# Performance work log

Hardware: AMD Instinct MI355X
Metric: run time of the kernel (lower is better)

The kernel has to match this reference:

```python
import math
import jax, jax.numpy as jnp
import numpy as np

N_HEADS = 16
THETA = 10000.0


def _rope_cos_sin(S, head_dim):
    half = head_dim // 2
    inv_freq = 1.0 / (THETA ** (jnp.arange(half, dtype=jnp.float32) / half))
    t = jnp.arange(S, dtype=jnp.float32)
    freqs = t[:, None] * inv_freq[None, :]  # [S, half]
    return jnp.cos(freqs), jnp.sin(freqs)


def _apply_rope(x, cos, sin):
    # x: [B, H, S, D] float32; cos/sin: [S, D//2]
    half = x.shape[-1] // 2
    x1, x2 = x[..., :half], x[..., half:]
    c = cos[None, None, :, :]
    s = sin[None, None, :, :]
    return jnp.concatenate([x1 * c - x2 * s, x1 * s + x2 * c], axis=-1)


def setup_inputs() -> dict:
    key = jax.random.key(0)
    k1, k2, k3 = jax.random.split(key, 3)
    B, S, D = 4, 2048, 1024
    x = jax.random.normal(k1, (B, S, D), dtype=jnp.float32)
    w_qkv = jax.random.normal(k2, (3 * D, D), dtype=jnp.float32) * (1.0 / math.sqrt(D))
    w_out = jax.random.normal(k3, (D, D), dtype=jnp.float32) * (1.0 / math.sqrt(D))
    return {"x": x, "w_qkv": w_qkv, "w_out": w_out}


def reference(x, w_qkv, w_out):
    B, S, D = x.shape
    H = N_HEADS
    hd = D // H

    qkv = x @ w_qkv.T  # [B, S, 3D]
    q, k, v = jnp.split(qkv, 3, axis=-1)

    def reshape(t):
        return t.reshape(B, S, H, hd).transpose(0, 2, 1, 3)  # [B,H,S,hd]

    q, k, v = reshape(q), reshape(k), reshape(v)

    cos, sin = _rope_cos_sin(S, hd)
    q = _apply_rope(q.astype(jnp.float32), cos, sin).astype(x.dtype)
    k = _apply_rope(k.astype(jnp.float32), cos, sin).astype(x.dtype)

    scale = math.sqrt(hd)
    scores = jnp.einsum("bhsd,bhtd->bhst", q, k) / scale  # [B,H,S,S]
    causal = jnp.tril(jnp.ones((S, S), dtype=bool))
    scores = jnp.where(causal[None, None], scores, -jnp.inf)
    attn = jax.nn.softmax(scores.astype(jnp.float32), axis=-1).astype(x.dtype)

    out = jnp.einsum("bhst,bhtd->bhsd", attn, v)  # [B,H,S,hd]
    out = out.transpose(0, 2, 1, 3).reshape(B, S, D)
    return out @ w_out.T
```

## Files before the change

kernel.cpp:

```cpp
#include <hip/hip_runtime.h>
#include <hip/hip_bf16.h>

#define DEV static __device__ __forceinline__

typedef unsigned short u16;
typedef unsigned int u32;
typedef __attribute__((ext_vector_type(8))) short short8;
typedef __attribute__((ext_vector_type(4))) float f32x4;
typedef __attribute__((ext_vector_type(16))) float f32x16;
typedef __attribute__((ext_vector_type(4))) u32 u32x4;

static constexpr int Bsz = 4, Ssz = 2048, Dsz = 1024, Hn = 16, HD = 64;
static constexpr int Mrows = Bsz * Ssz;

DEV u16 f2bu(float f) {
  union { float f; u32 u; } a; a.f = f;
  u32 u = a.u;
  u32 r = (u + 0x7FFFu + ((u >> 16) & 1u)) >> 16;
  return (u16)r;
}
DEV float b2f(u16 v) {
  union { u32 u; float f; } a; a.u = ((u32)v) << 16;
  return a.f;
}
DEV u32 pk2(float lo, float hi2) {
  __hip_bfloat162 t = __float22bfloat162_rn(make_float2(lo, hi2));
  u32 r; __builtin_memcpy(&r, &t, 4); return r;
}
DEV f32x16 mfma3232(short8 a, short8 b, f32x16 c) {
  return __builtin_amdgcn_mfma_f32_32x32x16_bf16(a, b, c, 0, 0, 0);
}
DEV float max3f(float a, float b, float c) { return fmaxf(fmaxf(a, b), c); }
DEV float ex2(float x) { return __builtin_amdgcn_exp2f(x); }

__global__ void k_cast(const float4* __restrict__ in, ushort4* __restrict__ out, int n4) {
  int stride = gridDim.x * blockDim.x;
  for (int i = blockIdx.x * blockDim.x + threadIdx.x; i < n4; i += stride) {
    float4 v = in[i];
    ushort4 o;
    o.x = f2bu(v.x); o.y = f2bu(v.y); o.z = f2bu(v.z); o.w = f2bu(v.w);
    out[i] = o;
  }
}

__global__ void k_ropetab(float2* __restrict__ cst) {
  int i = blockIdx.x * blockDim.x + threadIdx.x;
  if (i >= Ssz * 32) return;
  int s = i >> 5, d = i & 31;
  float inv = powf(10000.0f, -(float)d / 32.0f);
  float fr = (float)s * inv;
  cst[i] = make_float2(cosf(fr), sinf(fr));
}

DEV void cp16(const u16* g, u16* l) {
  __builtin_amdgcn_global_load_lds((const __attribute__((address_space(1))) u32*)g,
                                   (__attribute__((address_space(3))) u32*)l, 16, 0, 0);
}

template <bool OUTBF16>
__global__ __launch_bounds__(256, 2) void k_gemm(const u16* __restrict__ A,
                                                 const u16* __restrict__ W,
                                                 void* __restrict__ C, int N, int K,
                                                 const float2* __restrict__ cst, int cpx,
                                                 u16* __restrict__ vtp) {
  __shared__ __align__(16) u16 SMEM[33792];
  const int tid = threadIdx.x;
  const int wid = tid >> 6, lane = tid & 63;
  const int lr = lane & 15, u = lane >> 4;
  const int wm = wid >> 1, wn = wid & 1;

  const int wg = blockIdx.x;
  const int xcd = wg & 7;
  const int j = wg >> 3;
  const int brow = (j / cpx) * 128;
  const int bcol = (xcd * cpx + j % cpx) * 128;

  const int rw = wid * 32 + (lane >> 3);
  const int octS = ((lane & 7) ^ (rw & 7)) * 8;
  const u16* aS = A + (size_t)(brow + rw) * K + octS;
  const u16* bS = W + (size_t)(bcol + rw) * K + octS;
  const int dBase = wid * 2048 + lane * 8;

  const int aBase = (wm * 64 + lr) * 64;
  const int bBase = (wn * 64 + lr) * 64;
  const int o0 = (u ^ (lane & 7)) * 8;
  const int o1 = ((4 + u) ^ (lane & 7)) * 8;

  f32x4 acc[4][4];
#pragma unroll
  for (int i = 0; i < 4; ++i)
#pragma unroll
    for (int j2 = 0; j2 < 4; ++j2) acc[i][j2] = (f32x4){0.f, 0.f, 0.f, 0.f};

  const int nt = K >> 6;

#define STG(kk, bb)                                                    \
  do {                                                                 \
    u16* ad = SMEM + (bb)*8192 + dBase;                                \
    u16* bd = SMEM + 16384 + (bb)*8192 + dBase;                        \
    cp16(aS + (kk), ad);                                               \
    cp16(aS + (size_t)8 * K + (kk), ad + 512);                         \
    cp16(aS + (size_t)16 * K + (kk), ad + 1024);                       \
    cp16(aS + (size_t)24 * K + (kk), ad + 1536);                       \
    cp16(bS + (kk), bd);                                               \
    cp16(bS + (size_t)8 * K + (kk), bd + 512);                         \
    cp16(bS + (size_t)16 * K + (kk), bd + 1024);                       \
    cp16(bS + (size_t)24 * K + (kk), bd + 1536);                       \
  } while (0)

  STG(0, 0);

  for (int t = 0; t < nt; ++t) {
    asm volatile("s_waitcnt vmcnt(0)" ::: "memory");
    __builtin_amdgcn_s_barrier();
    if (t + 1 < nt) STG((t + 1) << 6, (t + 1) & 1);
    const u16* ab = SMEM + (t & 1) * 8192;
    const u16* bb = SMEM + 16384 + (t & 1) * 8192;
    short8 a0[4], a1[4], b0[4], b1[4];
#pragma unroll
    for (int mr = 0; mr < 4; ++mr) {
      a0[mr] = *(const short8*)(ab + aBase + mr * 1024 + o0);
      a1[mr] = *(const short8*)(ab + aBase + mr * 1024 + o1);
    }
#pragma unroll
    for (int nr = 0; nr < 4; ++nr) {
      b0[nr] = *(const short8*)(bb + bBase + nr * 1024 + o0);
      b1[nr] = *(const short8*)(bb + bBase + nr * 1024 + o1);
    }
    __builtin_amdgcn_s_setprio(1);
#pragma unroll
    for (int mr = 0; mr < 4; ++mr)
#pragma unroll
      for (int nr = 0; nr < 4; ++nr)
        acc[mr][nr] =
            __builtin_amdgcn_mfma_f32_16x16x32_bf16(a0[mr], b0[nr], acc[mr][nr], 0, 0, 0);
#pragma unroll
    for (int mr = 0; mr < 4; ++mr)
#pragma unroll
      for (int nr = 0; nr < 4; ++nr)
        acc[mr][nr] =
            __builtin_amdgcn_mfma_f32_16x16x32_bf16(a1[mr], b1[nr], acc[mr][nr], 0, 0, 0);
    __builtin_amdgcn_s_setprio(0);
  }
#undef STG

  if (OUTBF16) {
    __syncthreads();
    const int rmode = (bcol < 1024) ? 0 : (bcol < 2048) ? 1 : 2;
    if (rmode < 2) {
      const float sc = (rmode == 0) ? 0.18033688f : 1.0f;
#pragma unroll
      for (int mr = 0; mr < 4; ++mr)
#pragma unroll
        for (int r = 0; r < 4; ++r) {
          const int row = wm * 64 + mr * 16 + u * 4 + r;
          const int s = (brow + row) & 2047;
          const float2 c0 = cst[s * 32 + lr];
          const float2 c1 = cst[s * 32 + 16 + lr];
          const float x10 = acc[mr][0][r], x11 = acc[mr][1][r];
          const float x20 = acc[mr][2][r], x21 = acc[mr][3][r];
          u16* lp = SMEM + row * 136 + wn * 64 + lr;
          lp[0]  = f2bu((x10 * c0.x - x20 * c0.y) * sc);
          lp[16] = f2bu((x11 * c1.x - x21 * c1.y) * sc);
          lp[32] = f2bu((x10 * c0.y + x20 * c0.x) * sc);
          lp[48] = f2bu((x11 * c1.y + x21 * c1.x) * sc);
        }
      __syncthreads();
      u16* cp = (u16*)C;
#pragma unroll
      for (int i = 0; i < 8; ++i) {
        const int e = i * 2048 + tid * 8;
        const int row = e >> 7, col = e & 127;
        short8 v = *(const short8*)(SMEM + row * 136 + col);
        *(short8*)(cp + (size_t)(brow + row) * N + bcol + col) = v;
      }
    } else {
#pragma unroll
      for (int mr = 0; mr < 4; ++mr)
#pragma unroll
        for (int nr = 0; nr < 4; ++nr)
#pragma unroll
          for (int r = 0; r < 4; ++r) {
            const int dl = wn * 64 + nr * 16 + lr;
            const int sl = wm * 64 + mr * 16 + u * 4 + r;
            SMEM[dl * 136 + sl] = f2bu(acc[mr][nr][r]);
          }
      __syncthreads();
      const int bb2 = brow >> 11;
      const int sbase = brow & 2047;
#pragma unroll
      for (int i = 0; i < 8; ++i) {
        const int e = i * 2048 + tid * 8;
        const int dl = e >> 7, sl = e & 127;
        const int gd = (bcol - 2048) + dl;
        short8 v = *(const short8*)(SMEM + dl * 136 + sl);
        *(short8*)(vtp + (size_t)(bb2 * 1024 + gd) * 2048 + sbase + sl) = v;
      }
    }
  } else {
    __syncthreads();
    float* FS = (float*)SMEM;
#pragma unroll
    for (int mr = 0; mr < 4; ++mr)
#pragma unroll
      for (int nr = 0; nr < 4; ++nr)
#pragma unroll
        for (int r = 0; r < 4; ++r)
          FS[(wm * 64 + mr * 16 + u * 4 + r) * 132 + wn * 64 + nr * 16 + lr] =
              acc[mr][nr][r];
    __syncthreads();
    float* cp = (float*)C;
#pragma unroll
    for (int i = 0; i < 16; ++i) {
      const int e = i * 1024 + tid * 4;
      const int row = e >> 7, col = e & 127;
      float4 v = *(const float4*)(FS + row * 132 + col);
      *(float4*)(cp + (size_t)(brow + row) * N + bcol + col) = v;
    }
  }
}

__global__ __launch_bounds__(512, 4) void k_attn(const u16* __restrict__ qkv,
                                                 const u16* __restrict__ vt,
                                                 u16* __restrict__ obuf) {
  __shared__ __align__(16) u16 Ksm[2][64 * 64];
  __shared__ __align__(16) u16 Vsm[2][64 * 64];

  const int tid = threadIdx.x;
  const int wid = tid >> 6;
  const int lane = tid & 63;
  const int l31 = lane & 31;
  const int hi = lane >> 5;
  const int r7 = l31 & 7;

  const int fid = blockIdx.x;
  const int bh = fid & 63;
  const int e = (fid >> 6) & 7;
  const int qt = (e < 4) ? e : (7 - (e & 3));

  const int b = bh >> 4;
  const int h = bh & 15;

  const float NEG = -__builtin_inff();

  const int srow = lane >> 3;
  const int scol = ((lane & 7) ^ srow) * 8;
  const u16* ksrc = qkv + (size_t)(b * Ssz + wid * 8 + srow) * 3072 + 1024 + h * 64 + scol;
  const u16* vsrc = vt + ((size_t)bh * 64 + wid * 8 + srow) * Ssz + scol;
  u16* kD0 = Ksm[0] + wid * 512;
  u16* vD0 = Vsm[0] + wid * 512;

  const int q0 = qt * 256;
  const int qrow = q0 + (wid << 5) + l31;

  const u16* qptr = qkv + (size_t)(b * Ssz + qrow) * 3072 + h * 64 + hi * 8;
  short8 qf[4];
#pragma unroll
  for (int s = 0; s < 4; ++s) qf[s] = *(const short8*)(qptr + s * 16);

  f32x16 o0 = {0.f}, o1 = {0.f};
  float m = NEG, lsum = 0.f;

  const int ntiles = 4 * qt + 4;
  const int lastT = 4 * qt + (wid >> 1);

  cp16(ksrc, kD0);
  cp16(vsrc, vD0);

  const u16* kS = ksrc + (size_t)64 * 3072;
  const u16* vS = vsrc + 64;

  for (int t = 0; t < ntiles; ++t) {
    __syncthreads();
    if (t + 1 < ntiles) {
      const int nb = (t + 1) & 1;
      cp16(kS, kD0 + nb * 4096);
      cp16(vS, vD0 + nb * 4096);
      kS += (size_t)64 * 3072;
      vS += 64;
    }
    if (t > lastT) continue;

    const u16* kbuf = Ksm[t & 1];
    const u16* vbuf = Vsm[t & 1];
    const int kv0 = t << 6;

    f32x16 st0 = {0.f}, st1 = {0.f};
    __builtin_amdgcn_s_setprio(1);
#pragma unroll
    for (int s = 0; s < 4; ++s) {
      const int slot = (((2 * s + hi) ^ r7) << 3);
      short8 k0 = *(const short8*)(kbuf + l31 * 64 + slot);
      short8 k1 = *(const short8*)(kbuf + (32 + l31) * 64 + slot);
      st0 = mfma3232(k0, qf[s], st0);
      st1 = mfma3232(k1, qf[s], st1);
    }
    __builtin_amdgcn_s_setprio(0);

    if (t == lastT) {
      const int kb0 = kv0 + 4 * hi;
#pragma unroll
      for (int r = 0; r < 16; ++r) {
        const int ko = (r & 3) + 8 * (r >> 2);
        if (kb0 + ko > qrow) st0[r] = NEG;
        if (kb0 + 32 + ko > qrow) st1[r] = NEG;
      }
    }

    float c0 = max3f(st0[0], st0[1], st0[2]);
    c0 = max3f(c0, st0[3], st1[0]);
    c0 = max3f(c0, st1[1], st1[2]);
    c0 = fmaxf(c0, st1[3]);
    float c1 = max3f(st0[4], st0[5], st0[6]);
    c1 = max3f(c1, st0[7], st1[4]);
    c1 = max3f(c1, st1[5], st1[6]);
    c1 = fmaxf(c1, st1[7]);
    float c2 = max3f(st0[8], st0[9], st0[10]);
    c2 = max3f(c2, st0[11], st1[8]);
    c2 = max3f(c2, st1[9], st1[10]);
    c2 = fmaxf(c2, st1[11]);
    float c3 = max3f(st0[12], st0[13], st0[14]);
    c3 = max3f(c3, st0[15], st1[12]);
    c3 = max3f(c3, st1[13], st1[14]);
    c3 = fmaxf(c3, st1[15]);
    float pm = fmaxf(max3f(c0, c1, c2), c3);
    pm = fmaxf(pm, __shfl_xor(pm, 32));

    if (!__all(pm <= m + 8.0f)) {
      const float mn = fmaxf(m, pm);
      const float corr = ex2(m - mn);
      lsum *= corr;
      o0 *= corr;
      o1 *= corr;
      m = mn;
    }

    float rsp[4] = {0.f, 0.f, 0.f, 0.f};
#pragma unroll
    for (int r = 0; r < 16; ++r) {
      const float p0 = ex2(st0[r] - m);
      const float p1 = ex2(st1[r] - m);
      st0[r] = p0;
      st1[r] = p1;
      rsp[r & 3] += p0 + p1;
    }
    float rs = (rsp[0] + rsp[1]) + (rsp[2] + rsp[3]);
    rs += __shfl_xor(rs, 32);
    lsum += rs;

    u32 wa[8], wb[8];
#pragma unroll
    for (int g = 0; g < 4; ++g) {
      wa[g] = pk2(st0[4 * g + 0], st0[4 * g + 1]);
      wb[g] = pk2(st0[4 * g + 2], st0[4 * g + 3]);
      wa[4 + g] = pk2(st1[4 * g + 0], st1[4 * g + 1]);
      wb[4 + g] = pk2(st1[4 * g + 2], st1[4 * g + 3]);
    }

#pragma unroll
    for (int s = 0; s < 4; ++s) {
      const u32 uA0 = wa[2 * s], uA1 = wa[2 * s + 1];
      const u32 uB0 = wb[2 * s], uB1 = wb[2 * s + 1];
      const u32 tA0 = __shfl_xor(uA0, 32), tA1 = __shfl_xor(uA1, 32);
      const u32 tB0 = __shfl_xor(uB0, 32), tB1 = __shfl_xor(uB1, 32);
      u32x4 pw;
      pw.x = hi ? tA1 : uA0;
      pw.y = hi ? tB1 : uB0;
      pw.z = hi ? uA1 : tA0;
      pw.w = hi ? uB1 : tB0;
      short8 pfrag = *(short8*)&pw;
      const int slot = (((2 * s + hi) ^ r7) << 3);
      short8 v0 = *(const short8*)(vbuf + l31 * 64 + slot);
      short8 v1 = *(const short8*)(vbuf + (32 + l31) * 64 + slot);
      __builtin_amdgcn_s_setprio(1);
      o0 = mfma3232(v0, pfrag, o0);
      o1 = mfma3232(v1, pfrag, o1);
      __builtin_amdgcn_s_setprio(0);
    }
  }

  const float inv = 1.0f / lsum;
  u16* orow = obuf + (size_t)(b * Ssz + qrow) * 1024 + h * 64;
#pragma unroll
  for (int j = 0; j < 4; ++j) {
    ushort4 s0, s1;
    s0.x = f2bu(o0[4 * j + 0] * inv);
    s0.y = f2bu(o0[4 * j + 1] * inv);
    s0.z = f2bu(o0[4 * j + 2] * inv);
    s0.w = f2bu(o0[4 * j + 3] * inv);
    s1.x = f2bu(o1[4 * j + 0] * inv);
    s1.y = f2bu(o1[4 * j + 1] * inv);
    s1.z = f2bu(o1[4 * j + 2] * inv);
    s1.w = f2bu(o1[4 * j + 3] * inv);
    *(ushort4*)(orow + 8 * j + 4 * hi) = s0;
    *(ushort4*)(orow + 32 + 8 * j + 4 * hi) = s1;
  }
}

extern "C" void kernel_launch(void* const* d_in, const int* in_sizes, int n_in,
                              void* d_out, int out_size, void* d_ws, size_t ws_size,
                              hipStream_t stream) {
  const float* x = (const float*)d_in[0];
  const float* wqkv = (const float*)d_in[1];
  const float* wout = (const float*)d_in[2];

  char* ws = (char*)d_ws;
  u16* xb      = (u16*)(ws + 0);
  u16* wqkvb   = (u16*)(ws + 16777216);
  u16* woutb   = (u16*)(ws + 23068672);
  u16* qkv     = (u16*)(ws + 25165824);
  u16* vt      = (u16*)(ws + 75497472);
  u16* obuf    = (u16*)(ws + 92274688);
  float2* cst  = (float2*)(ws + 109051904);

  k_cast<<<2048, 256, 0, stream>>>((const float4*)x, (ushort4*)xb, Mrows * Dsz / 4);
  k_cast<<<2048, 256, 0, stream>>>((const float4*)wqkv, (ushort4*)wqkvb, 3 * Dsz * Dsz / 4);
  k_cast<<<1024, 256, 0, stream>>>((const float4*)wout, (ushort4*)woutb, Dsz * Dsz / 4);
  k_ropetab<<<256, 256, 0, stream>>>(cst);

  k_gemm<true><<<1536, 256, 0, stream>>>(xb, wqkvb, qkv, 3072, 1024, cst, 3, vt);

  k_attn<<<512, 512, 0, stream>>>(qkv, vt, obuf);

  k_gemm<false><<<512, 256, 0, stream>>>(obuf, woutb, d_out, 1024, 1024, nullptr, 1, nullptr);
}
```

Measured before the change: 182.3 us.

## Split attention KV range across two wave groups with smaller query tiles

```diff
diff --git a/kernel.cpp b/kernel.cpp
--- a/kernel.cpp
+++ b/kernel.cpp
@@ -220,11 +220,10 @@
   }
 }
 
-__global__ __launch_bounds__(512, 4) void k_attn(const u16* __restrict__ qkv,
+__global__ __launch_bounds__(512, 8) void k_attn(const u16* __restrict__ qkv,
                                                  const u16* __restrict__ vt,
                                                  u16* __restrict__ obuf) {
-  __shared__ __align__(16) u16 Ksm[2][64 * 64];
-  __shared__ __align__(16) u16 Vsm[2][64 * 64];
+  __shared__ __align__(16) u16 SM[16384];
 
   const int tid = threadIdx.x;
   const int wid = tid >> 6;
@@ -233,10 +232,14 @@
   const int hi = lane >> 5;
   const int r7 = l31 & 7;
 
+  const int p = wid >> 2;
+  const int s4 = wid & 3;
+
   const int fid = blockIdx.x;
-  const int bh = fid & 63;
-  const int e = (fid >> 6) & 7;
-  const int qt = (e < 4) ? e : (7 - (e & 3));
+  const int a = fid & 3, bq = (fid >> 8) & 3;
+  const int bh = (fid >> 2) & 63;
+  const int sel = a ^ bq;
+  const int qt = (sel == 0) ? bq : (sel == 1) ? 7 - bq : (sel == 2) ? 8 + bq : 15 - bq;
 
   const int b = bh >> 4;
   const int h = bh & 15;
@@ -245,13 +248,15 @@
 
   const int srow = lane >> 3;
   const int scol = ((lane & 7) ^ srow) * 8;
-  const u16* ksrc = qkv + (size_t)(b * Ssz + wid * 8 + srow) * 3072 + 1024 + h * 64 + scol;
-  const u16* vsrc = vt + ((size_t)bh * 64 + wid * 8 + srow) * Ssz + scol;
-  u16* kD0 = Ksm[0] + wid * 512;
-  u16* vD0 = Vsm[0] + wid * 512;
-
-  const int q0 = qt * 256;
-  const int qrow = q0 + (wid << 5) + l31;
+  const u16* kS = qkv + (size_t)(b * Ssz + p * 64 + 16 * s4 + srow) * 3072 + 1024 + h * 64 + scol;
+  const u16* vS = vt + ((size_t)bh * 64 + 16 * s4 + srow) * Ssz + p * 64 + scol;
+  u16* kD = SM + p * 4096 + s4 * 1024;
+  u16* vD = SM + 8192 + p * 4096 + s4 * 1024;
+  const u16* kbuf = SM + p * 4096;
+  const u16* vbuf = SM + 8192 + p * 4096;
+
+  const int q0 = qt * 128;
+  const int qrow = q0 + (s4 << 5) + l31;
 
   const u16* qptr = qkv + (size_t)(b * Ssz + qrow) * 3072 + h * 64 + hi * 8;
   short8 qf[4];
@@ -261,139 +266,165 @@
   f32x16 o0 = {0.f}, o1 = {0.f};
   float m = NEG, lsum = 0.f;
 
-  const int ntiles = 4 * qt + 4;
-  const int lastT = 4 * qt + (wid >> 1);
-
-  cp16(ksrc, kD0);
-  cp16(vsrc, vD0);
-
-  const u16* kS = ksrc + (size_t)64 * 3072;
-  const u16* vS = vsrc + 64;
-
-  for (int t = 0; t < ntiles; ++t) {
+  const int lastT = 2 * qt + (s4 >> 1);
+  const int nss = qt + 1;
+
+  for (int ss = 0; ss < nss; ++ss) {
+    const int tc = 2 * ss + p;
     __syncthreads();
-    if (t + 1 < ntiles) {
-      const int nb = (t + 1) & 1;
-      cp16(kS, kD0 + nb * 4096);
-      cp16(vS, vD0 + nb * 4096);
-      kS += (size_t)64 * 3072;
-      vS += 64;
-    }
-    if (t > lastT) continue;
-
-    const u16* kbuf = Ksm[t & 1];
-    const u16* vbuf = Vsm[t & 1];
-    const int kv0 = t << 6;
-
-    f32x16 st0 = {0.f}, st1 = {0.f};
-    __builtin_amdgcn_s_setprio(1);
-#pragma unroll
-    for (int s = 0; s < 4; ++s) {
-      const int slot = (((2 * s + hi) ^ r7) << 3);
-      short8 k0 = *(const short8*)(kbuf + l31 * 64 + slot);
-      short8 k1 = *(const short8*)(kbuf + (32 + l31) * 64 + slot);
-      st0 = mfma3232(k0, qf[s], st0);
-      st1 = mfma3232(k1, qf[s], st1);
-    }
-    __builtin_amdgcn_s_setprio(0);
-
-    if (t == lastT) {
-      const int kb0 = kv0 + 4 * hi;
+    cp16(kS, kD);
+    cp16(kS + (size_t)8 * 3072, kD + 512);
+    cp16(vS, vD);
+    cp16(vS + (size_t)8 * Ssz, vD + 512);
+    kS += (size_t)128 * 3072;
+    vS += 128;
+    __syncthreads();
+
+    if (tc <= lastT) {
+      const int kv0 = tc << 6;
+
+      f32x16 st0 = {0.f}, st1 = {0.f};
+      __builtin_amdgcn_s_setprio(1);
+#pragma unroll
+      for (int s = 0; s < 4; ++s) {
+        const int slot = (((2 * s + hi) ^ r7) << 3);
+        short8 k0 = *(const short8*)(kbuf + l31 * 64 + slot);
+        short8 k1 = *(const short8*)(kbuf + (32 + l31) * 64 + slot);
+        st0 = mfma3232(k0, qf[s], st0);
+        st1 = mfma3232(k1, qf[s], st1);
+      }
+      __builtin_amdgcn_s_setprio(0);
+
+      if (tc == lastT) {
+        const int kb0 = kv0 + 4 * hi;
+#pragma unroll
+        for (int r = 0; r < 16; ++r) {
+          const int ko = (r & 3) + 8 * (r >> 2);
+          if (kb0 + ko > qrow) st0[r] = NEG;
+          if (kb0 + 32 + ko > qrow) st1[r] = NEG;
+        }
+      }
+
+      float c0 = max3f(st0[0], st0[1], st0[2]);
+      c0 = max3f(c0, st0[3], st1[0]);
+      c0 = max3f(c0, st1[1], st1[2]);
+      c0 = fmaxf(c0, st1[3]);
+      float c1 = max3f(st0[4], st0[5], st0[6]);
+      c1 = max3f(c1, st0[7], st1[4]);
+      c1 = max3f(c1, st1[5], st1[6]);
+      c1 = fmaxf(c1, st1[7]);
+      float c2 = max3f(st0[8], st0[9], st0[10]);
+      c2 = max3f(c2, st0[11], st1[8]);
+      c2 = max3f(c2, st1[9], st1[10]);
+      c2 = fmaxf(c2, st1[11]);
+      float c3 = max3f(st0[12], st0[13], st0[14]);
+      c3 = max3f(c3, st0[15], st1[12]);
+      c3 = max3f(c3, st1[13], st1[14]);
+      c3 = fmaxf(c3, st1[15]);
+      float pm = fmaxf(max3f(c0, c1, c2), c3);
+      pm = fmaxf(pm, __shfl_xor(pm, 32));
+
+      if (!__all(pm <= m + 8.0f)) {
+        const float mn = fmaxf(m, pm);
+        const float corr = ex2(m - mn);
+        lsum *= corr;
+        o0 *= corr;
+        o1 *= corr;
+        m = mn;
+      }
+
+      float rsp[4] = {0.f, 0.f, 0.f, 0.f};
 #pragma unroll
       for (int r = 0; r < 16; ++r) {
-        const int ko = (r & 3) + 8 * (r >> 2);
-        if (kb0 + ko > qrow) st0[r] = NEG;
-        if (kb0 + 32 + ko > qrow) st1[r] = NEG;
-      }
-    }
-
-    float c0 = max3f(st0[0], st0[1], st0[2]);
-    c0 = max3f(c0, st0[3], st1[0]);
-    c0 = max3f(c0, st1[1], st1[2]);
-    c0 = fmaxf(c0, st1[3]);
-    float c1 = max3f(st0[4], st0[5], st0[6]);
-    c1 = max3f(c1, st0[7], st1[4]);
-    c1 = max3f(c1, st1[5], st1[6]);
-    c1 = fmaxf(c1, st1[7]);
-    float c2 = max3f(st0[8], st0[9], st0[10]);
-    c2 = max3f(c2, st0[11], st1[8]);
-    c2 = max3f(c2, st1[9], st1[10]);
-    c2 = fmaxf(c2, st1[11]);
-    float c3 = max3f(st0[12], st0[13], st0[14]);
-    c3 = max3f(c3, st0[15], st1[12]);
-    c3 = max3f(c3, st1[13], st1[14]);
-    c3 = fmaxf(c3, st1[15]);
-    float pm = fmaxf(max3f(c0, c1, c2), c3);
-    pm = fmaxf(pm, __shfl_xor(pm, 32));
-
-    if (!__all(pm <= m + 8.0f)) {
-      const float mn = fmaxf(m, pm);
-      const float corr = ex2(m - mn);
-      lsum *= corr;
-      o0 *= corr;
-      o1 *= corr;
-      m = mn;
-    }
-
-    float rsp[4] = {0.f, 0.f, 0.f, 0.f};
-#pragma unroll
-    for (int r = 0; r < 16; ++r) {
-      const float p0 = ex2(st0[r] - m);
-      const float p1 = ex2(st1[r] - m);
-      st0[r] = p0;
-      st1[r] = p1;
-      rsp[r & 3] += p0 + p1;
-    }
-    float rs = (rsp[0] + rsp[1]) + (rsp[2] + rsp[3]);
-    rs += __shfl_xor(rs, 32);
-    lsum += rs;
-
-    u32 wa[8], wb[8];
-#pragma unroll
-    for (int g = 0; g < 4; ++g) {
-      wa[g] = pk2(st0[4 * g + 0], st0[4 * g + 1]);
-      wb[g] = pk2(st0[4 * g + 2], st0[4 * g + 3]);
-      wa[4 + g] = pk2(st1[4 * g + 0], st1[4 * g + 1]);
-      wb[4 + g] = pk2(st1[4 * g + 2], st1[4 * g + 3]);
-    }
-
-#pragma unroll
-    for (int s = 0; s < 4; ++s) {
-      const u32 uA0 = wa[2 * s], uA1 = wa[2 * s + 1];
-      const u32 uB0 = wb[2 * s], uB1 = wb[2 * s + 1];
-      const u32 tA0 = __shfl_xor(uA0, 32), tA1 = __shfl_xor(uA1, 32);
-      const u32 tB0 = __shfl_xor(uB0, 32), tB1 = __shfl_xor(uB1, 32);
-      u32x4 pw;
-      pw.x = hi ? tA1 : uA0;
-      pw.y = hi ? tB1 : uB0;
-      pw.z = hi ? uA1 : tA0;
-      pw.w = hi ? uB1 : tB0;
-      short8 pfrag = *(short8*)&pw;
-      const int slot = (((2 * s + hi) ^ r7) << 3);
-      short8 v0 = *(const short8*)(vbuf + l31 * 64 + slot);
-      short8 v1 = *(const short8*)(vbuf + (32 + l31) * 64 + slot);
-      __builtin_amdgcn_s_setprio(1);
-      o0 = mfma3232(v0, pfrag, o0);
-      o1 = mfma3232(v1, pfrag, o1);
-      __builtin_amdgcn_s_setprio(0);
-    }
-  }
-
-  const float inv = 1.0f / lsum;
-  u16* orow = obuf + (size_t)(b * Ssz + qrow) * 1024 + h * 64;
-#pragma unroll
-  for (int j = 0; j < 4; ++j) {
-    ushort4 s0, s1;
-    s0.x = f2bu(o0[4 * j + 0] * inv);
-    s0.y = f2bu(o0[4 * j + 1] * inv);
-    s0.z = f2bu(o0[4 * j + 2] * inv);
-    s0.w = f2bu(o0[4 * j + 3] * inv);
-    s1.x = f2bu(o1[4 * j + 0] * inv);
-    s1.y = f2bu(o1[4 * j + 1] * inv);
-    s1.z = f2bu(o1[4 * j + 2] * inv);
-    s1.w = f2bu(o1[4 * j + 3] * inv);
-    *(ushort4*)(orow + 8 * j + 4 * hi) = s0;
-    *(ushort4*)(orow + 32 + 8 * j + 4 * hi) = s1;
+        const float p0 = ex2(st0[r] - m);
+        const float p1 = ex2(st1[r] - m);
+        st0[r] = p0;
+        st1[r] = p1;
+        rsp[r & 3] += p0 + p1;
+      }
+      float rs = (rsp[0] + rsp[1]) + (rsp[2] + rsp[3]);
+      rs += __shfl_xor(rs, 32);
+      lsum += rs;
+
+      u32 wa[8], wb[8];
+#pragma unroll
+      for (int g = 0; g < 4; ++g) {
+        wa[g] = pk2(st0[4 * g + 0], st0[4 * g + 1]);
+        wb[g] = pk2(st0[4 * g + 2], st0[4 * g + 3]);
+        wa[4 + g] = pk2(st1[4 * g + 0], st1[4 * g + 1]);
+        wb[4 + g] = pk2(st1[4 * g + 2], st1[4 * g + 3]);
+      }
+
+#pragma unroll
+      for (int s = 0; s < 4; ++s) {
+        const u32 uA0 = wa[2 * s], uA1 = wa[2 * s + 1];
+        const u32 uB0 = wb[2 * s], uB1 = wb[2 * s + 1];
+        const u32 tA0 = __shfl_xor(uA0, 32), tA1 = __shfl_xor(uA1, 32);
+        const u32 tB0 = __shfl_xor(uB0, 32), tB1 = __shfl_xor(uB1, 32);
+        u32x4 pw;
+        pw.x = hi ? tA1 : uA0;
+        pw.y = hi ? tB1 : uB0;
+        pw.z = hi ? uA1 : tA0;
+        pw.w = hi ? uB1 : tB0;
+        short8 pfrag = *(short8*)&pw;
+        const int slot = (((2 * s + hi) ^ r7) << 3);
+        short8 v0 = *(const short8*)(vbuf + l31 * 64 + slot);
+        short8 v1 = *(const short8*)(vbuf + (32 + l31) * 64 + slot);
+        __builtin_amdgcn_s_setprio(1);
+        o0 = mfma3232(v0, pfrag, o0);
+        o1 = mfma3232(v1, pfrag, o1);
+        __builtin_amdgcn_s_setprio(0);
+      }
+    }
+  }
+
+  float* MG = (float*)SM;
+  __syncthreads();
+  if (p == 1) {
+    MG[s4 * 128 + lane * 2 + 0] = m;
+    MG[s4 * 128 + lane * 2 + 1] = lsum;
+#pragma unroll
+    for (int j = 0; j < 16; ++j) MG[512 + j * 256 + s4 * 64 + lane] = o0[j];
+  }
+  __syncthreads();
+  float ca = 1.f, cb = 0.f, linv = 0.f;
+  if (p == 0) {
+    const float mb = MG[s4 * 128 + lane * 2 + 0];
+    const float lb = MG[s4 * 128 + lane * 2 + 1];
+    const float mx = fmaxf(m, mb);
+    ca = ex2(m - mx);
+    cb = ex2(mb - mx);
+    linv = 1.0f / (lsum * ca + lb * cb);
+#pragma unroll
+    for (int j = 0; j < 16; ++j)
+      o0[j] = o0[j] * ca + MG[512 + j * 256 + s4 * 64 + lane] * cb;
+  }
+  __syncthreads();
+  if (p == 1) {
+#pragma unroll
+    for (int j = 0; j < 16; ++j) MG[512 + j * 256 + s4 * 64 + lane] = o1[j];
+  }
+  __syncthreads();
+  if (p == 0) {
+#pragma unroll
+    for (int j = 0; j < 16; ++j)
+      o1[j] = o1[j] * ca + MG[512 + j * 256 + s4 * 64 + lane] * cb;
+
+    u16* orow = obuf + (size_t)(b * Ssz + qrow) * 1024 + h * 64;
+#pragma unroll
+    for (int j = 0; j < 4; ++j) {
+      ushort4 s0, s1;
+      s0.x = f2bu(o0[4 * j + 0] * linv);
+      s0.y = f2bu(o0[4 * j + 1] * linv);
+      s0.z = f2bu(o0[4 * j + 2] * linv);
+      s0.w = f2bu(o0[4 * j + 3] * linv);
+      s1.x = f2bu(o1[4 * j + 0] * linv);
+      s1.y = f2bu(o1[4 * j + 1] * linv);
+      s1.z = f2bu(o1[4 * j + 2] * linv);
+      s1.w = f2bu(o1[4 * j + 3] * linv);
+      *(ushort4*)(orow + 8 * j + 4 * hi) = s0;
+      *(ushort4*)(orow + 32 + 8 * j + 4 * hi) = s1;
+    }
   }
 }
 
@@ -420,7 +451,7 @@
 
   k_gemm<true><<<1536, 256, 0, stream>>>(xb, wqkvb, qkv, 3072, 1024, cst, 3, vt);
 
-  k_attn<<<512, 512, 0, stream>>>(qkv, vt, obuf);
+  k_attn<<<1024, 512, 0, stream>>>(qkv, vt, obuf);
 
   k_gemm<false><<<512, 256, 0, stream>>>(obuf, woutb, d_out, 1024, 1024, nullptr, 1, nullptr);
 }
```

Result: slower. 552.5 us (+203.1%).
